# Kernel tuning notes

Hardware: AMD Instinct MI355X
Metric: run time of the kernel (lower is better)

Reference implementation:

```python
import jax, jax.numpy as jnp
import numpy as np

# Module config (mirrors PlateYoloBlock __init__)
IMAGE_W, IMAGE_H = 2048, 2048
GRID_SIZE = 8
GRID_W = IMAGE_W // GRID_SIZE  # 256
GRID_H = IMAGE_H // GRID_SIZE  # 256
BBOX_ATTRS = 13


def _xy_offset():
    # np.meshgrid(arange(grid_w), arange(grid_h)) stacked on axis=2 -> (grid_h, grid_w, 2)
    # [..., 0] = x (column) index, [..., 1] = y (row) index
    gx = jnp.arange(GRID_W, dtype=jnp.float32)
    gy = jnp.arange(GRID_H, dtype=jnp.float32)
    xx, yy = jnp.meshgrid(gx, gy)  # each (grid_h, grid_w)
    return jnp.stack([xx, yy], axis=-1)  # (grid_h, grid_w, 2)


def setup_inputs() -> dict:
    key = jax.random.key(0)
    coordinates = jax.random.normal(key, (32, BBOX_ATTRS, GRID_H, GRID_W), dtype=jnp.float32)
    return {"coordinates": coordinates}


def reference(coordinates) -> jnp.ndarray:
    # Inference path of PlateYoloBlock.forward (target=None):
    #   permute (B,13,H,W) -> (B,H,W,13)
    #   xy   = sigmoid(raw[..., :2]) + grid offset
    #   wh   = exp(raw[..., 2:4])
    #   conf = sigmoid(raw[..., -1])
    #   all-but-conf scaled by grid_size; reshape to (B, grid_w*grid_h, 13)
    b = coordinates.shape[0]
    c = jnp.transpose(coordinates, (0, 2, 3, 1))  # (B, grid_h, grid_w, 13)
    xy = jax.nn.sigmoid(c[..., :2]) + _xy_offset()[None]  # (B,H,W,2)
    wh = jnp.exp(c[..., 2:4])
    corners = c[..., 4:12]  # raw 4-corner coords, untouched by activations
    conf = jax.nn.sigmoid(c[..., 12:13])
    boxes = jnp.concatenate([xy, wh, corners], axis=-1) * jnp.float32(GRID_SIZE)
    out = jnp.concatenate([boxes, conf], axis=-1)  # (B,H,W,13)
    return out.reshape(b, GRID_W * GRID_H, BBOX_ATTRS)
```

## Files before the change

kernel.cpp:

```cpp
#include <hip/hip_runtime.h>


#define NB      32
#define NC      13
#define HW      65536
#define WIDTH   256
#define TILE    1024
#define THREADS 256

__device__ __forceinline__ float sigmoidf_(float x) {
    return 1.0f / (1.0f + __expf(-x));
}

__global__ __launch_bounds__(THREADS) void plate_yolo_kernel(
        const float* __restrict__ in, float* __restrict__ out) {
    const int tid = threadIdx.x;
    const long long s0 = (long long)blockIdx.x * TILE;
    const int b = (int)(s0 >> 16);
    const int posBase = (int)(s0 & (HW - 1));
    const float* __restrict__ inB = in + (long long)b * NC * HW + posBase;

    const int p4 = tid * 4;
    float4 v[NC];
    #pragma unroll
    for (int c = 0; c < NC; ++c)
        v[c] = *(const float4*)(inB + c * HW + p4);

    const int pos = posBase + p4;
    const float fx0 = (float)(pos & (WIDTH - 1));
    const float fy  = (float)(pos >> 8);

    __align__(16) float o[4 * NC];
    #pragma unroll
    for (int j = 0; j < 4; ++j) {
        const float x = fx0 + (float)j;
        #pragma unroll
        for (int c = 0; c < NC; ++c) {
            const float val = ((const float*)&v[c])[j];
            float r;
            if (c == 0)                 r = (sigmoidf_(val) + x) * 8.0f;
            else if (c == 1)            r = (sigmoidf_(val) + fy) * 8.0f;
            else if (c == 2 || c == 3)  r = __expf(val) * 8.0f;
            else if (c == 12)           r = sigmoidf_(val);
            else                        r = val * 8.0f;
            o[j * NC + c] = r;
        }
    }

    float4* __restrict__ dst = (float4*)(out + s0 * NC + (long long)tid * (4 * NC));
    #pragma unroll
    for (int q = 0; q < NC; ++q)
        dst[q] = *(const float4*)&o[4 * q];
}

extern "C" void kernel_launch(void* const* d_in, const int* in_sizes, int n_in,
                              void* d_out, int out_size, void* d_ws, size_t ws_size,
                              hipStream_t stream) {
    const float* in = (const float*)d_in[0];
    float* out = (float*)d_out;
    const int blocks = (NB * HW) / TILE;
    plate_yolo_kernel<<<blocks, THREADS, 0, stream>>>(in, out);
}
```

Baseline: 224.5 us.

## Stage output tile in per-wave LDS for coalesced global stores

Each wave now writes its interleaved 13-attribute results into a private LDS slab, then stores the slab to global memory with lane-contiguous float4 writes. Before, each thread wrote a 208-byte stride, so stores were scattered across many cache lines. Blocks shrink to two waves, and each wave handles two 256-position tiles in turn. The change relies on wave-level lockstep with no explicit barrier, and it adds an extra LDS round trip.

New measurement: 194.0 us. -13.6%, faster.

```diff
diff --git a/kernel.cpp b/kernel.cpp
--- a/kernel.cpp
+++ b/kernel.cpp
@@ -5,8 +5,10 @@
 #define NC      13
 #define HW      65536
 #define WIDTH   256
-#define TILE    1024
-#define THREADS 256
+#define WTILE   256
+#define TPW     2
+#define WAVES   2
+#define THREADS (WAVES * 64)
 
 __device__ __forceinline__ float sigmoidf_(float x) {
     return 1.0f / (1.0f + __expf(-x));
@@ -14,43 +16,57 @@
 
 __global__ __launch_bounds__(THREADS) void plate_yolo_kernel(
         const float* __restrict__ in, float* __restrict__ out) {
-    const int tid = threadIdx.x;
-    const long long s0 = (long long)blockIdx.x * TILE;
-    const int b = (int)(s0 >> 16);
-    const int posBase = (int)(s0 & (HW - 1));
-    const float* __restrict__ inB = in + (long long)b * NC * HW + posBase;
+    __shared__ __align__(16) float lds[WAVES][WTILE * NC];
 
-    const int p4 = tid * 4;
-    float4 v[NC];
+    const int lane = threadIdx.x & 63;
+    const int wid  = threadIdx.x >> 6;
+    float* slab = lds[wid];
+
     #pragma unroll
-    for (int c = 0; c < NC; ++c)
-        v[c] = *(const float4*)(inB + c * HW + p4);
+    for (int s = 0; s < TPW; ++s) {
+        const int T = blockIdx.x * (WAVES * TPW) + wid * TPW + s;
+        const int b = T >> 8;
+        const int posBase = (T & 255) * WTILE;
+        const float* __restrict__ inB = in + (size_t)b * NC * HW + posBase;
+        const int p4 = lane * 4;
 
-    const int pos = posBase + p4;
-    const float fx0 = (float)(pos & (WIDTH - 1));
-    const float fy  = (float)(pos >> 8);
+        float4 v[NC];
+        #pragma unroll
+        for (int c = 0; c < NC; ++c)
+            v[c] = *(const float4*)(inB + c * HW + p4);
 
-    __align__(16) float o[4 * NC];
-    #pragma unroll
-    for (int j = 0; j < 4; ++j) {
-        const float x = fx0 + (float)j;
+        const int pos = posBase + p4;
+        const float fx0 = (float)(pos & (WIDTH - 1));
+        const float fy  = (float)(pos >> 8);
+
+        __align__(16) float o[4 * NC];
         #pragma unroll
-        for (int c = 0; c < NC; ++c) {
-            const float val = ((const float*)&v[c])[j];
-            float r;
-            if (c == 0)                 r = (sigmoidf_(val) + x) * 8.0f;
-            else if (c == 1)            r = (sigmoidf_(val) + fy) * 8.0f;
-            else if (c == 2 || c == 3)  r = __expf(val) * 8.0f;
-            else if (c == 12)           r = sigmoidf_(val);
-            else                        r = val * 8.0f;
-            o[j * NC + c] = r;
+        for (int j = 0; j < 4; ++j) {
+            const float x = fx0 + (float)j;
+            #pragma unroll
+            for (int c = 0; c < NC; ++c) {
+                const float val = ((const float*)&v[c])[j];
+                float r;
+                if (c == 0)                 r = (sigmoidf_(val) + x) * 8.0f;
+                else if (c == 1)            r = (sigmoidf_(val) + fy) * 8.0f;
+                else if (c == 2 || c == 3)  r = __expf(val) * 8.0f;
+                else if (c == 12)           r = sigmoidf_(val);
+                else                        r = val * 8.0f;
+                o[j * NC + c] = r;
+            }
         }
+
+        float4* wslab = (float4*)(slab + lane * (4 * NC));
+        #pragma unroll
+        for (int q = 0; q < NC; ++q)
+            wslab[q] = *(const float4*)&o[4 * q];
+
+        const float4* __restrict__ src = (const float4*)slab;
+        float4* __restrict__ dst = (float4*)(out + (size_t)T * (WTILE * NC));
+        #pragma unroll
+        for (int q = 0; q < NC; ++q)
+            dst[q * 64 + lane] = src[q * 64 + lane];
     }
-
-    float4* __restrict__ dst = (float4*)(out + s0 * NC + (long long)tid * (4 * NC));
-    #pragma unroll
-    for (int q = 0; q < NC; ++q)
-        dst[q] = *(const float4*)&o[4 * q];
 }
 
 extern "C" void kernel_launch(void* const* d_in, const int* in_sizes, int n_in,
@@ -58,6 +74,6 @@
                               hipStream_t stream) {
     const float* in = (const float*)d_in[0];
     float* out = (float*)d_out;
-    const int blocks = (NB * HW) / TILE;
+    const int blocks = (NB * HW / WTILE) / (WAVES * TPW);
     plate_yolo_kernel<<<blocks, THREADS, 0, stream>>>(in, out);
 }
```
